# Optimization experiments

Hardware: AMD Instinct MI355X
Metric: run time of the kernel (lower is better)

## Reference

```python
import jax, jax.numpy as jnp
import numpy as np

K_NEIGHBORS = 16
BN_EPS = 1e-5


def _bn(h, g, b):
    # train-mode BatchNorm1d over (batch, points) per channel, biased variance
    mu = h.mean(axis=(0, 1))
    var = h.var(axis=(0, 1))
    return g * (h - mu) * jax.lax.rsqrt(var + BN_EPS) + b


def _gather(arr, idx):
    # arr: [B,N,D], idx: [B,N,K] -> [B,N,K,D]
    return jax.vmap(lambda a, i: a[i])(arr, idx)


def setup_inputs() -> dict:
    key = jax.random.key(0)
    ks = jax.random.split(key, 16)
    B, N, Cin, C, H, M = 4, 4096, 64, 64, 32, 4
    rn = lambda k, s: jax.random.normal(k, s, dtype=jnp.float32) * 0.05
    return {
        "x": jax.random.normal(ks[0], (B, N, Cin), dtype=jnp.float32),
        "p": jax.random.normal(ks[1], (B, N, 3), dtype=jnp.float32),
        "fc1_w": rn(ks[2], (Cin, C)), "fc1_b": jnp.zeros((C,), jnp.float32),
        "bn1_g": jnp.ones((C,), jnp.float32), "bn1_b": jnp.zeros((C,), jnp.float32),
        "qkv_w": rn(ks[3], (C, 3 * C)),
        "pos_w1": rn(ks[4], (3, H)), "pos_b1": jnp.zeros((H,), jnp.float32),
        "pos_w2": rn(ks[5], (H, C)), "pos_b2": jnp.zeros((C,), jnp.float32),
        "attn_w1": rn(ks[6], (C, M * C)), "attn_b1": jnp.zeros((M * C,), jnp.float32),
        "attn_w2": rn(ks[7], (M * C, C)), "attn_b2": jnp.zeros((C,), jnp.float32),
        "bn2_g": jnp.ones((C,), jnp.float32), "bn2_b": jnp.zeros((C,), jnp.float32),
        "fc2_w": rn(ks[8], (C, C)), "fc2_b": jnp.zeros((C,), jnp.float32),
        "bn3_g": jnp.ones((C,), jnp.float32), "bn3_b": jnp.zeros((C,), jnp.float32),
    }


def reference(x, p, fc1_w, fc1_b, bn1_g, bn1_b, qkv_w,
              pos_w1, pos_b1, pos_w2, pos_b2,
              attn_w1, attn_b1, attn_w2, attn_b2,
              bn2_g, bn2_b, fc2_w, fc2_b, bn3_g, bn3_b):
    C = fc1_w.shape[1]
    # fc1 -> BN -> ReLU
    h = jax.nn.relu(_bn(x @ fc1_w + fc1_b, bn1_g, bn1_b))
    residual = h

    # PointTransformerLayer (vector attention over kNN; mask is all-ones)
    qkv = h @ qkv_w  # [B,N,3C]
    q, k, v = qkv[..., :C], qkv[..., C:2 * C], qkv[..., 2 * C:]
    # squared pairwise distances (matches norm-based topk ranking)
    sq = jnp.sum(p * p, axis=-1)  # [B,N]
    d2 = sq[:, :, None] + sq[:, None, :] - 2.0 * jnp.einsum('bnd,bmd->bnm', p, p)
    _, idx = jax.lax.top_k(-d2, K_NEIGHBORS)  # k smallest distances, [B,N,K]

    kj = _gather(k, idx)          # [B,N,K,C]
    vj = _gather(v, idx)          # [B,N,K,C]
    pj = _gather(p, idx)          # [B,N,K,3]

    rel_pos = p[:, :, None, :] - pj                      # [B,N,K,3]
    pe = jax.nn.relu(rel_pos @ pos_w1 + pos_b1) @ pos_w2 + pos_b2  # [B,N,K,C]

    qk_rel = q[:, :, None, :] - kj                       # [B,N,K,C]
    vv = vj + pe
    sim = jax.nn.relu((qk_rel + pe) @ attn_w1 + attn_b1) @ attn_w2 + attn_b2
    attn = jax.nn.softmax(sim, axis=2)                   # softmax over neighbors
    agg = jnp.sum(attn * vv, axis=2)                     # [B,N,C]

    h2 = jax.nn.relu(_bn(agg, bn2_g, bn2_b))
    y = jax.nn.relu(_bn((h2 + residual) @ fc2_w + fc2_b, bn3_g, bn3_b))
    return (y, p)
```

## Files before the change

kernel.cpp:

```cpp
#include <hip/hip_runtime.h>
#include <math.h>

constexpr int kB = 4, kN = 4096, kK = 16;
constexpr int kRows = kB * kN;
constexpr float kEps = 1e-5f;
constexpr float kFltMax = 3.402823466e38f;
constexpr int kCap = 240;

typedef __attribute__((ext_vector_type(8))) short short8;
typedef __attribute__((ext_vector_type(4))) float f32x4;

__device__ __forceinline__ unsigned short f2bf(float x) {
  return (unsigned short)((__float_as_uint(x) + 0x8000u) >> 16);
}
__device__ __forceinline__ unsigned int pkbf(float lo, float hi) {
  return ((__float_as_uint(lo) + 0x8000u) >> 16) |
         ((__float_as_uint(hi) + 0x8000u) & 0xffff0000u);
}
__device__ __forceinline__ short8 pack8f(float4 a, float4 b) {
  union { unsigned int u[4]; short8 s; } pk;
  pk.u[0] = pkbf(a.x, a.y);
  pk.u[1] = pkbf(a.z, a.w);
  pk.u[2] = pkbf(b.x, b.y);
  pk.u[3] = pkbf(b.z, b.w);
  return pk.s;
}

__device__ __forceinline__ int lane_prefix(unsigned long long m) {
  return __builtin_amdgcn_mbcnt_hi((unsigned)(m >> 32),
         __builtin_amdgcn_mbcnt_lo((unsigned)m, 0));
}

__device__ __forceinline__ void bitonic64(float& sv, int& si, int lane) {
  #pragma unroll
  for (int k = 2; k <= 64; k <<= 1) {
    #pragma unroll
    for (int j = k >> 1; j > 0; j >>= 1) {
      float ov = __shfl_xor(sv, j);
      int   oi = __shfl_xor(si, j);
      bool up = ((lane & k) == 0);
      bool lower = ((lane & j) == 0);
      bool osm = (ov < sv) || (ov == sv && oi < si);
      bool take = (lower == up) ? osm : !osm;
      if (take) { sv = ov; si = oi; }
    }
  }
}

__global__ __launch_bounds__(256) void fc1_conv_kernel(
    const float* __restrict__ x, const float* __restrict__ w,
    const float* __restrict__ bias,
    const float* __restrict__ aw1, const float* __restrict__ aw2,
    const float* __restrict__ pw2, const float* __restrict__ qw,
    const float* __restrict__ f2w,
    const float* __restrict__ pin, float* __restrict__ p4o,
    unsigned short* __restrict__ wpak,
    float* __restrict__ out) {
  __shared__ unsigned short wf[8 * 512];
  const int t = threadIdx.x;
  const int blk = blockIdx.x;
  {
    int id = blk * 256 + t;
    if (id < 16384) {
      int j = id & 7, lane = (id >> 3) & 63, rest = id >> 9;
      int mt = rest >> 1, hh = rest & 1;
      wpak[id] = f2bf(aw1[(32 * hh + 8 * (lane >> 4) + j) * 256 + mt * 16 + (lane & 15)]);
      float3 pp = *reinterpret_cast<const float3*>(pin + 3 * id);
      float4 o;
      o.x = pp.x; o.y = pp.y; o.z = pp.z;
      o.w = pp.x * pp.x + pp.y * pp.y + pp.z * pp.z;
      *reinterpret_cast<float4*>(p4o + 4 * id) = o;
    } else if (id < 32768) {
      int i = id - 16384;
      int j = i & 7, lane = (i >> 3) & 63, rest = i >> 9;
      int ct = rest >> 3, f = rest & 7;
      wpak[id] = f2bf(aw2[(32 * f + 8 * (lane >> 4) + j) * 64 + ct * 16 + (lane & 15)]);
    } else if (id < 34816) {
      int i = id - 32768;
      int c = i >> 5, hh = i & 31;
      wpak[id] = f2bf(pw2[hh * 64 + c]);
    } else if (id < 47104) {
      int i = id - 34816;
      int j = i & 7, lane = (i >> 3) & 63, rest = i >> 9;
      int ct = rest >> 1, hh = rest & 1;
      wpak[id] = f2bf(qw[(32 * hh + 8 * (lane >> 4) + j) * 192 + ct * 16 + (lane & 15)]);
    } else if (id < 51200) {
      int i = id - 47104;
      int j = i & 7, lane = (i >> 3) & 63, rest = i >> 9;
      int ct = rest >> 1, hh = rest & 1;
      wpak[id] = f2bf(f2w[(32 * hh + 8 * (lane >> 4) + j) * 64 + ct * 16 + (lane & 15)]);
    }
  }
  for (int i = t; i < 4096; i += 256) {
    int j = i & 7, lane = (i >> 3) & 63, rest = i >> 9;
    int ct = rest >> 1, hh = rest & 1;
    wf[i] = f2bf(w[(32 * hh + 8 * (lane >> 4) + j) * 64 + ct * 16 + (lane & 15)]);
  }
  __syncthreads();
  const int lane = t & 63, wv = t >> 6;
  const int l = lane & 15, q = lane >> 4;
  const int r0 = blk * 64;
  const int row = r0 + wv * 16 + l;
  const f32x4 zero = {0.f, 0.f, 0.f, 0.f};
  float4 xa0 = *reinterpret_cast<const float4*>(&x[row * 64 + q * 8]);
  float4 xa1 = *reinterpret_cast<const float4*>(&x[row * 64 + q * 8 + 4]);
  float4 xb0 = *reinterpret_cast<const float4*>(&x[row * 64 + 32 + q * 8]);
  float4 xb1 = *reinterpret_cast<const float4*>(&x[row * 64 + 32 + q * 8 + 4]);
  short8 a0 = pack8f(xa0, xa1), a1 = pack8f(xb0, xb1);
  #pragma unroll
  for (int ct = 0; ct < 4; ++ct) {
    short8 b0 = *reinterpret_cast<const short8*>(&wf[(ct * 2 + 0) * 512 + lane * 8]);
    short8 b1 = *reinterpret_cast<const short8*>(&wf[(ct * 2 + 1) * 512 + lane * 8]);
    f32x4 acc = __builtin_amdgcn_mfma_f32_16x16x32_bf16(a0, b0, zero, 0, 0, 0);
    acc = __builtin_amdgcn_mfma_f32_16x16x32_bf16(a1, b1, acc, 0, 0, 0);
    const float bc = bias[ct * 16 + l];
    #pragma unroll
    for (int i = 0; i < 4; ++i)
      out[(r0 + wv * 16 + q * 4 + i) * 64 + ct * 16 + l] = acc[i] + bc;
  }
}

__global__ void stats_part_kernel(const float* __restrict__ src, float* __restrict__ part) {
  __shared__ float sb[256], sb2[256];
  const int t = threadIdx.x, blk = blockIdx.x;
  const int c = t & 63, rg = t >> 6;
  float s = 0.f, s2 = 0.f;
  for (int r = rg; r < 64; r += 4) {
    float v = src[(blk * 64 + r) * 64 + c];
    s += v; s2 += v * v;
  }
  sb[t] = s; sb2[t] = s2; __syncthreads();
  if (t < 64) {
    float ts  = sb[t] + sb[64 + t] + sb[128 + t] + sb[192 + t];
    float ts2 = sb2[t] + sb2[64 + t] + sb2[128 + t] + sb2[192 + t];
    part[blk * 128 + t] = ts;
    part[blk * 128 + 64 + t] = ts2;
  }
}

__global__ void stats_fin_kernel(const float* __restrict__ part,
                                 const float* __restrict__ g, const float* __restrict__ b,
                                 float* __restrict__ A, float* __restrict__ Bv) {
  const int c = threadIdx.x;
  double s = 0.0, s2 = 0.0;
  for (int i = 0; i < 256; ++i) { s += part[i * 128 + c]; s2 += part[i * 128 + 64 + c]; }
  double mean = s / (double)kRows;
  double var = s2 / (double)kRows - mean * mean;
  float rs = (float)(1.0 / sqrt(var + (double)kEps));
  float Af = g[c] * rs;
  A[c] = Af;
  Bv[c] = b[c] - (float)mean * Af;
}

__global__ __launch_bounds__(256) void qkv_bn_kernel(
    const float* __restrict__ hpre, const float* __restrict__ A1,
    const float* __restrict__ B1, const unsigned short* __restrict__ wqf,
    float* __restrict__ hout, unsigned short* __restrict__ out) {
  const int t = threadIdx.x, lane = t & 63, wv = t >> 6;
  const int l = lane & 15, q = lane >> 4;
  const int r0 = blockIdx.x * 64;
  const int row = r0 + wv * 16 + l;
  const f32x4 zero = {0.f, 0.f, 0.f, 0.f};
  short8 af[2];
  #pragma unroll
  for (int hh = 0; hh < 2; ++hh) {
    const int c0 = 32 * hh + q * 8;
    float4 v0 = *reinterpret_cast<const float4*>(&hpre[row * 64 + c0]);
    float4 v1 = *reinterpret_cast<const float4*>(&hpre[row * 64 + c0 + 4]);
    float4 Aa = *reinterpret_cast<const float4*>(&A1[c0]);
    float4 Ab = *reinterpret_cast<const float4*>(&A1[c0 + 4]);
    float4 Ba = *reinterpret_cast<const float4*>(&B1[c0]);
    float4 Bb = *reinterpret_cast<const float4*>(&B1[c0 + 4]);
    v0.x = fmaxf(Aa.x * v0.x + Ba.x, 0.f); v0.y = fmaxf(Aa.y * v0.y + Ba.y, 0.f);
    v0.z = fmaxf(Aa.z * v0.z + Ba.z, 0.f); v0.w = fmaxf(Aa.w * v0.w + Ba.w, 0.f);
    v1.x = fmaxf(Ab.x * v1.x + Bb.x, 0.f); v1.y = fmaxf(Ab.y * v1.y + Bb.y, 0.f);
    v1.z = fmaxf(Ab.z * v1.z + Bb.z, 0.f); v1.w = fmaxf(Ab.w * v1.w + Bb.w, 0.f);
    *reinterpret_cast<float4*>(&hout[row * 64 + c0]) = v0;
    *reinterpret_cast<float4*>(&hout[row * 64 + c0 + 4]) = v1;
    af[hh] = pack8f(v0, v1);
  }
  #pragma unroll
  for (int ct = 0; ct < 12; ++ct) {
    short8 b0 = *reinterpret_cast<const short8*>(&wqf[((ct * 2 + 0) * 64 + lane) * 8]);
    short8 b1 = *reinterpret_cast<const short8*>(&wqf[((ct * 2 + 1) * 64 + lane) * 8]);
    f32x4 acc = __builtin_amdgcn_mfma_f32_16x16x32_bf16(af[0], b0, zero, 0, 0, 0);
    acc = __builtin_amdgcn_mfma_f32_16x16x32_bf16(af[1], b1, acc, 0, 0, 0);
    #pragma unroll
    for (int i = 0; i < 4; ++i)
      out[(r0 + wv * 16 + q * 4 + i) * 192 + ct * 16 + l] = f2bf(acc[i]);
  }
}

__global__ __launch_bounds__(256) void knn_attn_kernel(
    const float* __restrict__ p4, const unsigned short* __restrict__ qkv,
    const float* __restrict__ pos_w1, const float* __restrict__ pos_b1,
    const float* __restrict__ pos_b2,
    const float* __restrict__ attn_b1, const float* __restrict__ attn_b2,
    const unsigned short* __restrict__ w1f,
    const unsigned short* __restrict__ w2f,
    const unsigned short* __restrict__ pw2t,
    float* __restrict__ agg) {
  __shared__ unsigned short Ulds[64 * 72];
  __shared__ float VVlds[64 * 68];
  __shared__ int   knnidx[4][kCap];

  const int t = threadIdx.x;
  const int lane = t & 63, w = t >> 6;
  const int l = lane & 15, q = lane >> 4;
  const int work = ((blockIdx.x & 7) << 9) | (blockIdx.x >> 3);
  const int b = work >> 10;
  const int pt_row = work * 4 + w;
  const int base = b * kN;
  const f32x4 zero = {0.f, 0.f, 0.f, 0.f};

  int* bufi = knnidx[w];

  const float4 qp4 = *reinterpret_cast<const float4*>(p4 + 4 * pt_row);
  const float qx = qp4.x, qy = qp4.y, qz = qp4.z, sqq = qp4.w;

  float d2r[16];
  float lmin = kFltMax;
  #pragma unroll
  for (int i = 0; i < 16; ++i) {
    float4 c = *reinterpret_cast<const float4*>(p4 + 4 * (base + i * 64 + lane));
    float dot = fmaf(qz, c.z, fmaf(qy, c.y, qx * c.x));
    float d2 = fmaf(-2.0f, dot, sqq + c.w);
    d2r[i] = d2;
    lmin = fminf(lmin, d2);
  }
  { int dummy = lane; bitonic64(lmin, dummy, lane); }
  const float thrA = __shfl(lmin, 15) + 1e-3f;

  int cntv = 0;
  #pragma unroll
  for (int i = 0; i < 16; ++i) {
    bool qual = d2r[i] <= thrA;
    unsigned long long m = __ballot(qual);
    if (qual) {
      int pos = cntv + lane_prefix(m);
      if (pos < kCap) bufi[pos] = i * 64 + lane;
    }
    cntv += __popcll(m);
  }
  for (int c0 = 16; c0 < 64; c0 += 8) {
    float4 cc[8];
    #pragma unroll
    for (int j = 0; j < 8; ++j)
      cc[j] = *reinterpret_cast<const float4*>(p4 + 4 * (base + (c0 + j) * 64 + lane));
    #pragma unroll
    for (int j = 0; j < 8; ++j) {
      float dot = fmaf(qz, cc[j].z, fmaf(qy, cc[j].y, qx * cc[j].x));
      float d2 = fmaf(-2.0f, dot, sqq + cc[j].w);
      bool qual = d2 <= thrA;
      unsigned long long m = __ballot(qual);
      if (qual) {
        int pos = cntv + lane_prefix(m);
        if (pos < kCap) bufi[pos] = (c0 + j) * 64 + lane;
      }
      cntv += __popcll(m);
    }
  }

  const int n = cntv;
  float sv = kFltMax;
  int   si = 0x7fffffff;
  if (n <= kCap) {
    for (int g0 = 0; g0 < n; g0 += 48) {
      float mv; int mi;
      if (lane < 16) { mv = sv; mi = si; }
      else {
        int pos = g0 + (lane - 16);
        if (pos < n) {
          int jj = bufi[pos];
          float4 c = *reinterpret_cast<const float4*>(p4 + 4 * (base + jj));
          float dot = fmaf(qz, c.z, fmaf(qy, c.y, qx * c.x));
          mv = fmaf(-2.0f, dot, sqq + c.w);
          mi = jj;
        } else { mv = kFltMax; mi = 0x7fffffff; }
      }
      bitonic64(mv, mi, lane);
      sv = mv; si = mi;
    }
  } else {
    for (int g0 = 0; g0 < kN; g0 += 48) {
      float mv; int mi;
      if (lane < 16) { mv = sv; mi = si; }
      else {
        int j = g0 + (lane - 16);
        if (j < kN) {
          float4 c = *reinterpret_cast<const float4*>(p4 + 4 * (base + j));
          float dot = fmaf(qz, c.z, fmaf(qy, c.y, qx * c.x));
          mv = fmaf(-2.0f, dot, sqq + c.w);
          mi = j;
        } else { mv = kFltMax; mi = 0x7fffffff; }
      }
      bitonic64(mv, mi, lane);
      sv = mv; si = mi;
    }
  }

  int idxv = 0;
  if (lane < 16) {
    int o = si;
    if ((unsigned)o >= (unsigned)kN) o = 0;
    idxv = o;
  }

  {
    const int r = lane >> 2, seg = lane & 3;
    const unsigned short* jrow = qkv + (base + __shfl(idxv, r)) * 192;
    const int c0 = seg * 16;
    uint4 k0 = *reinterpret_cast<const uint4*>(jrow + 64 + c0);
    uint4 k1 = *reinterpret_cast<const uint4*>(jrow + 64 + c0 + 8);
    uint4 v0 = *reinterpret_cast<const uint4*>(jrow + 128 + c0);
    uint4 v1 = *reinterpret_cast<const uint4*>(jrow + 128 + c0 + 8);
    uint4 q0 = *reinterpret_cast<const uint4*>(qkv + pt_row * 192 + c0);
    uint4 q1 = *reinterpret_cast<const uint4*>(qkv + pt_row * 192 + c0 + 8);
    auto diff2 = [](unsigned int qu, unsigned int ku) -> unsigned int {
      float lo = __uint_as_float(qu << 16) - __uint_as_float(ku << 16);
      float hi = __uint_as_float(qu & 0xffff0000u) - __uint_as_float(ku & 0xffff0000u);
      return pkbf(lo, hi);
    };
    uint4 u0, u1;
    u0.x = diff2(q0.x, k0.x); u0.y = diff2(q0.y, k0.y);
    u0.z = diff2(q0.z, k0.z); u0.w = diff2(q0.w, k0.w);
    u1.x = diff2(q1.x, k1.x); u1.y = diff2(q1.y, k1.y);
    u1.z = diff2(q1.z, k1.z); u1.w = diff2(q1.w, k1.w);
    *reinterpret_cast<uint4*>(&Ulds[(w * 16 + r) * 72 + c0]) = u0;
    *reinterpret_cast<uint4*>(&Ulds[(w * 16 + r) * 72 + c0 + 8]) = u1;
    const unsigned int vs[8] = {v0.x, v0.y, v0.z, v0.w, v1.x, v1.y, v1.z, v1.w};
    #pragma unroll
    for (int i = 0; i < 4; ++i) {
      float4 vv;
      vv.x = __uint_as_float(vs[2 * i] << 16);
      vv.y = __uint_as_float(vs[2 * i] & 0xffff0000u);
      vv.z = __uint_as_float(vs[2 * i + 1] << 16);
      vv.w = __uint_as_float(vs[2 * i + 1] & 0xffff0000u);
      *reinterpret_cast<float4*>(&VVlds[(w * 16 + r) * 68 + c0 + 4 * i]) = vv;
    }
  }
  short8 pbf;
  {
    const int nj = __shfl(idxv, l);
    const float4 pj4 = *reinterpret_cast<const float4*>(p4 + 4 * (base + nj));
    float rx = qx - pj4.x, ry = qy - pj4.y, rz = qz - pj4.z;
    float hv[8];
    #pragma unroll
    for (int j = 0; j < 8; ++j) {
      int hh = q * 8 + j;
      hv[j] = fmaxf(pos_b1[hh] + rx * pos_w1[hh] + ry * pos_w1[32 + hh] +
                    rz * pos_w1[64 + hh], 0.0f);
    }
    union { unsigned int u[4]; short8 s; } pk;
    #pragma unroll
    for (int ii = 0; ii < 4; ++ii) pk.u[ii] = pkbf(hv[2 * ii], hv[2 * ii + 1]);
    pbf = pk.s;
  }

  {
    const int urow = (w * 16 + l) * 72;
    const int vrow = (w * 16 + l) * 68;
    #pragma unroll
    for (int mt = 0; mt < 4; ++mt) {
      short8 paf = *reinterpret_cast<const short8*>(&pw2t[(mt * 16 + l) * 32 + q * 8]);
      f32x4 pe = __builtin_amdgcn_mfma_f32_16x16x32_bf16(paf, pbf, zero, 0, 0, 0);
      const int c0 = mt * 16 + q * 4;
      float4 b2v = *reinterpret_cast<const float4*>(&pos_b2[c0]);
      float pe0 = pe[0] + b2v.x, pe1 = pe[1] + b2v.y;
      float pe2 = pe[2] + b2v.z, pe3 = pe[3] + b2v.w;
      uint2 u2 = *reinterpret_cast<uint2*>(&Ulds[urow + c0]);
      uint2 o;
      o.x = pkbf(__uint_as_float(u2.x << 16) + pe0,
                 __uint_as_float(u2.x & 0xffff0000u) + pe1);
      o.y = pkbf(__uint_as_float(u2.y << 16) + pe2,
                 __uint_as_float(u2.y & 0xffff0000u) + pe3);
      *reinterpret_cast<uint2*>(&Ulds[urow + c0]) = o;
      float4 vv = *reinterpret_cast<float4*>(&VVlds[vrow + c0]);
      vv.x += pe0; vv.y += pe1; vv.z += pe2; vv.w += pe3;
      *reinterpret_cast<float4*>(&VVlds[vrow + c0]) = vv;
    }
  }

  unsigned int plo[16], phi[16];
  {
    const int urow = (w * 16 + l) * 72;
    short8 ub0 = *reinterpret_cast<const short8*>(&Ulds[urow + q * 8]);
    short8 ub1 = *reinterpret_cast<const short8*>(&Ulds[urow + 32 + q * 8]);
    #pragma unroll
    for (int mt = 0; mt < 16; ++mt) {
      short8 a0 = *reinterpret_cast<const short8*>(&w1f[(mt * 2 + 0) * 512 + lane * 8]);
      short8 a1 = *reinterpret_cast<const short8*>(&w1f[(mt * 2 + 1) * 512 + lane * 8]);
      f32x4 acc = __builtin_amdgcn_mfma_f32_16x16x32_bf16(a0, ub0, zero, 0, 0, 0);
      acc = __builtin_amdgcn_mfma_f32_16x16x32_bf16(a1, ub1, acc, 0, 0, 0);
      float4 bb = *reinterpret_cast<const float4*>(&attn_b1[mt * 16 + q * 4]);
      plo[mt] = pkbf(fmaxf(acc[0] + bb.x, 0.f), fmaxf(acc[1] + bb.y, 0.f));
      phi[mt] = pkbf(fmaxf(acc[2] + bb.z, 0.f), fmaxf(acc[3] + bb.w, 0.f));
    }
  }

  {
    f32x4 acc2[4];
    #pragma unroll
    for (int ct = 0; ct < 4; ++ct) acc2[ct] = zero;
    const int sbase = l + 32 * (q & 1);
    const bool hi_mt = (q >= 2);
    #pragma unroll
    for (int f = 0; f < 8; ++f) {
      union { unsigned int u[4]; short8 s; } pk;
      #pragma unroll
      for (int d = 0; d < 4; ++d) {
        const int src = sbase + ((d >> 1) << 4);
        const unsigned int w0 = (d & 1) ? phi[2 * f] : plo[2 * f];
        const unsigned int w1v = (d & 1) ? phi[2 * f + 1] : plo[2 * f + 1];
        unsigned int va = (unsigned int)__shfl((int)w0, src);
        unsigned int vb = (unsigned int)__shfl((int)w1v, src);
        pk.u[d] = hi_mt ? vb : va;
      }
      short8 afr = pk.s;
      #pragma unroll
      for (int ct = 0; ct < 4; ++ct) {
        short8 bfr = *reinterpret_cast<const short8*>(&w2f[((ct * 8 + f) * 64 + lane) * 8]);
        acc2[ct] = __builtin_amdgcn_mfma_f32_16x16x32_bf16(afr, bfr, acc2[ct], 0, 0, 0);
      }
    }
    #pragma unroll
    for (int ct = 0; ct < 4; ++ct) {
      const int ch = ct * 16 + l;
      const float bv = attn_b2[ch];
      float s0v = acc2[ct][0] + bv, s1v = acc2[ct][1] + bv;
      float s2v = acc2[ct][2] + bv, s3v = acc2[ct][3] + bv;
      float mx = fmaxf(fmaxf(s0v, s1v), fmaxf(s2v, s3v));
      mx = fmaxf(mx, __shfl_xor(mx, 16, 64));
      mx = fmaxf(mx, __shfl_xor(mx, 32, 64));
      float e0 = __expf(s0v - mx), e1 = __expf(s1v - mx);
      float e2 = __expf(s2v - mx), e3 = __expf(s3v - mx);
      float se = e0 + e1 + e2 + e3;
      se += __shfl_xor(se, 16, 64);
      se += __shfl_xor(se, 32, 64);
      const int vbase = (w * 16 + q * 4) * 68 + ch;
      float a = e0 * VVlds[vbase] + e1 * VVlds[vbase + 68] +
                e2 * VVlds[vbase + 136] + e3 * VVlds[vbase + 204];
      a += __shfl_xor(a, 16, 64);
      a += __shfl_xor(a, 32, 64);
      if (q == 0) agg[pt_row * 64 + ch] = a / se;
    }
  }
}

__global__ __launch_bounds__(256) void fc2_mfma_kernel(
    const float* __restrict__ aggp, const float* __restrict__ hres,
    const float* __restrict__ A2, const float* __restrict__ B2,
    const unsigned short* __restrict__ fc2f, const float* __restrict__ bias,
    float* __restrict__ z) {
  const int t = threadIdx.x, lane = t & 63, wv = t >> 6;
  const int l = lane & 15, q = lane >> 4;
  const int r0 = blockIdx.x * 64;
  const int row = r0 + wv * 16 + l;
  const f32x4 zero = {0.f, 0.f, 0.f, 0.f};
  short8 af[2];
  #pragma unroll
  for (int hh = 0; hh < 2; ++hh) {
    const int c0 = 32 * hh + q * 8;
    float4 v0 = *reinterpret_cast<const float4*>(&aggp[row * 64 + c0]);
    float4 v1 = *reinterpret_cast<const float4*>(&aggp[row * 64 + c0 + 4]);
    float4 r0v = *reinterpret_cast<const float4*>(&hres[row * 64 + c0]);
    float4 r1v = *reinterpret_cast<const float4*>(&hres[row * 64 + c0 + 4]);
    float4 Aa = *reinterpret_cast<const float4*>(&A2[c0]);
    float4 Ab = *reinterpret_cast<const float4*>(&A2[c0 + 4]);
    float4 Ba = *reinterpret_cast<const float4*>(&B2[c0]);
    float4 Bb = *reinterpret_cast<const float4*>(&B2[c0 + 4]);
    v0.x = fmaxf(Aa.x * v0.x + Ba.x, 0.f) + r0v.x;
    v0.y = fmaxf(Aa.y * v0.y + Ba.y, 0.f) + r0v.y;
    v0.z = fmaxf(Aa.z * v0.z + Ba.z, 0.f) + r0v.z;
    v0.w = fmaxf(Aa.w * v0.w + Ba.w, 0.f) + r0v.w;
    v1.x = fmaxf(Ab.x * v1.x + Bb.x, 0.f) + r1v.x;
    v1.y = fmaxf(Ab.y * v1.y + Bb.y, 0.f) + r1v.y;
    v1.z = fmaxf(Ab.z * v1.z + Bb.z, 0.f) + r1v.z;
    v1.w = fmaxf(Ab.w * v1.w + Bb.w, 0.f) + r1v.w;
    af[hh] = pack8f(v0, v1);
  }
  #pragma unroll
  for (int ct = 0; ct < 4; ++ct) {
    short8 b0 = *reinterpret_cast<const short8*>(&fc2f[((ct * 2 + 0) * 64 + lane) * 8]);
    short8 b1 = *reinterpret_cast<const short8*>(&fc2f[((ct * 2 + 1) * 64 + lane) * 8]);
    f32x4 acc = __builtin_amdgcn_mfma_f32_16x16x32_bf16(af[0], b0, zero, 0, 0, 0);
    acc = __builtin_amdgcn_mfma_f32_16x16x32_bf16(af[1], b1, acc, 0, 0, 0);
    const float bc = bias[ct * 16 + l];
    #pragma unroll
    for (int i = 0; i < 4; ++i)
      z[(r0 + wv * 16 + q * 4 + i) * 64 + ct * 16 + l] = acc[i] + bc;
  }
}

__global__ void final_kernel(const float* __restrict__ z, const float* __restrict__ A3,
                             const float* __restrict__ B3, const float* __restrict__ p,
                             float* __restrict__ y) {
  const int blk = blockIdx.x, t = threadIdx.x;
  if (blk < 4096) {
    int i = blk * 256 + t;
    int c = i & 63;
    y[i] = fmaxf(A3[c] * z[i] + B3[c], 0.0f);
  } else {
    int i = (blk - 4096) * 256 + t;
    y[1048576 + i] = p[i];
  }
}

extern "C" void kernel_launch(void* const* d_in, const int* in_sizes, int n_in,
                              void* d_out, int out_size, void* d_ws, size_t ws_size,
                              hipStream_t stream) {
  const float* x       = (const float*)d_in[0];
  const float* p       = (const float*)d_in[1];
  const float* fc1_w   = (const float*)d_in[2];
  const float* fc1_b   = (const float*)d_in[3];
  const float* bn1_g   = (const float*)d_in[4];
  const float* bn1_b   = (const float*)d_in[5];
  const float* qkv_w   = (const float*)d_in[6];
  const float* pos_w1  = (const float*)d_in[7];
  const float* pos_b1  = (const float*)d_in[8];
  const float* pos_w2  = (const float*)d_in[9];
  const float* pos_b2  = (const float*)d_in[10];
  const float* attn_w1 = (const float*)d_in[11];
  const float* attn_b1 = (const float*)d_in[12];
  const float* attn_w2 = (const float*)d_in[13];
  const float* attn_b2 = (const float*)d_in[14];
  const float* bn2_g   = (const float*)d_in[15];
  const float* bn2_b   = (const float*)d_in[16];
  const float* fc2_w   = (const float*)d_in[17];
  const float* fc2_b   = (const float*)d_in[18];
  const float* bn3_g   = (const float*)d_in[19];
  const float* bn3_b   = (const float*)d_in[20];

  float* ws   = (float*)d_ws;
  float* h    = ws;
  unsigned short* qkvb = (unsigned short*)(ws + 1048576);
  float* hpre = ws + 4194304;
  float* aggv = ws + 5242880;
  float* z    = ws + 6291456;
  float* st   = ws + 7340032;
  float* p4   = ws + 7356800;
  unsigned short* wpak = (unsigned short*)(ws + 7618944);
  unsigned short* w1f  = wpak;
  unsigned short* w2f  = wpak + 16384;
  unsigned short* pw2t = wpak + 32768;
  unsigned short* wqf  = wpak + 34816;
  unsigned short* fc2f = wpak + 47104;

  float* A1 = st,       *B1 = st + 64;
  float* A2 = st + 128, *B2 = st + 192;
  float* A3 = st + 256, *B3 = st + 320;
  float* y = (float*)d_out;

  fc1_conv_kernel<<<256, 256, 0, stream>>>(x, fc1_w, fc1_b, attn_w1, attn_w2,
                                           pos_w2, qkv_w, fc2_w, p, p4, wpak, hpre);
  stats_part_kernel<<<256, 256, 0, stream>>>(hpre, aggv);
  stats_fin_kernel<<<1, 64, 0, stream>>>(aggv, bn1_g, bn1_b, A1, B1);
  qkv_bn_kernel<<<256, 256, 0, stream>>>(hpre, A1, B1, wqf, h, qkvb);
  knn_attn_kernel<<<4096, 256, 0, stream>>>(p4, qkvb, pos_w1, pos_b1, pos_b2,
                                            attn_b1, attn_b2, w1f, w2f, pw2t, aggv);
  stats_part_kernel<<<256, 256, 0, stream>>>(aggv, z);
  stats_fin_kernel<<<1, 64, 0, stream>>>(z, bn2_g, bn2_b, A2, B2);
  fc2_mfma_kernel<<<256, 256, 0, stream>>>(aggv, h, A2, B2, fc2f, fc2_b, z);
  stats_part_kernel<<<256, 256, 0, stream>>>(z, aggv);
  stats_fin_kernel<<<1, 64, 0, stream>>>(aggv, bn3_g, bn3_b, A3, B3);
  final_kernel<<<4288, 256, 0, stream>>>(z, A3, B3, p, y);
}
```

Baseline: 284.0 us.

## Share kNN candidate scan across block waves, building per-query lists cooperatively

Each wave now loads only a quarter of the batch's points and computes distances to all four queries in the block. It keeps bf16-truncated distances in registers, and the per-wave thresholds are exchanged through shared memory. Candidate lists are then appended with LDS atomics into reused VVlds space. This cuts the redundant per-wave global loads of the whole point cloud by four times. The trade-off is a looser threshold taken from a subset, which means more candidates to refine and a higher chance of overflowing the cap. It also adds extra syncs and atomics.

```diff
diff --git a/kernel.cpp b/kernel.cpp
--- a/kernel.cpp
+++ b/kernel.cpp
@@ -202,7 +202,8 @@
     float* __restrict__ agg) {
   __shared__ unsigned short Ulds[64 * 72];
   __shared__ float VVlds[64 * 68];
-  __shared__ int   knnidx[4][kCap];
+  __shared__ int   scnt[4];
+  __shared__ float sthr[4];
 
   const int t = threadIdx.x;
   const int lane = t & 63, w = t >> 6;
@@ -210,58 +211,99 @@
   const int work = ((blockIdx.x & 7) << 9) | (blockIdx.x >> 3);
   const int b = work >> 10;
   const int pt_row = work * 4 + w;
+  const int qrow0 = work * 4;
   const int base = b * kN;
   const f32x4 zero = {0.f, 0.f, 0.f, 0.f};
 
-  int* bufi = knnidx[w];
-
+  if (t < 4) scnt[t] = 0;
+
+  const float4 q0f = *reinterpret_cast<const float4*>(p4 + 4 * (qrow0 + 0));
+  const float4 q1f = *reinterpret_cast<const float4*>(p4 + 4 * (qrow0 + 1));
+  const float4 q2f = *reinterpret_cast<const float4*>(p4 + 4 * (qrow0 + 2));
+  const float4 q3f = *reinterpret_cast<const float4*>(p4 + 4 * (qrow0 + 3));
   const float4 qp4 = *reinterpret_cast<const float4*>(p4 + 4 * pt_row);
   const float qx = qp4.x, qy = qp4.y, qz = qp4.z, sqq = qp4.w;
 
-  float d2r[16];
+  auto d2q = [](const float4& Q, const float4& C) -> float {
+    float dt = fmaf(Q.z, C.z, fmaf(Q.y, C.y, Q.x * C.x));
+    return fmaf(-2.0f, dt, Q.w + C.w);
+  };
+  unsigned pk0[8], pk1[8], pk2[8], pk3[8];
   float lmin = kFltMax;
+  const int cbase = base + w * 1024;
   #pragma unroll
-  for (int i = 0; i < 16; ++i) {
-    float4 c = *reinterpret_cast<const float4*>(p4 + 4 * (base + i * 64 + lane));
-    float dot = fmaf(qz, c.z, fmaf(qy, c.y, qx * c.x));
-    float d2 = fmaf(-2.0f, dot, sqq + c.w);
-    d2r[i] = d2;
-    lmin = fminf(lmin, d2);
-  }
-  { int dummy = lane; bitonic64(lmin, dummy, lane); }
-  const float thrA = __shfl(lmin, 15) + 1e-3f;
-
-  int cntv = 0;
-  #pragma unroll
-  for (int i = 0; i < 16; ++i) {
-    bool qual = d2r[i] <= thrA;
-    unsigned long long m = __ballot(qual);
-    if (qual) {
-      int pos = cntv + lane_prefix(m);
-      if (pos < kCap) bufi[pos] = i * 64 + lane;
-    }
-    cntv += __popcll(m);
-  }
-  for (int c0 = 16; c0 < 64; c0 += 8) {
+  for (int g = 0; g < 2; ++g) {
     float4 cc[8];
     #pragma unroll
-    for (int j = 0; j < 8; ++j)
-      cc[j] = *reinterpret_cast<const float4*>(p4 + 4 * (base + (c0 + j) * 64 + lane));
-    #pragma unroll
-    for (int j = 0; j < 8; ++j) {
-      float dot = fmaf(qz, cc[j].z, fmaf(qy, cc[j].y, qx * cc[j].x));
-      float d2 = fmaf(-2.0f, dot, sqq + cc[j].w);
-      bool qual = d2 <= thrA;
-      unsigned long long m = __ballot(qual);
-      if (qual) {
-        int pos = cntv + lane_prefix(m);
-        if (pos < kCap) bufi[pos] = (c0 + j) * 64 + lane;
+    for (int jj = 0; jj < 8; ++jj)
+      cc[jj] = *reinterpret_cast<const float4*>(p4 + 4 * (cbase + (g * 8 + jj) * 64 + lane));
+    #pragma unroll
+    for (int jj = 0; jj < 8; ++jj) {
+      float dot = fmaf(qz, cc[jj].z, fmaf(qy, cc[jj].y, qx * cc[jj].x));
+      lmin = fminf(lmin, fmaf(-2.0f, dot, sqq + cc[jj].w));
+    }
+    #pragma unroll
+    for (int pi = 0; pi < 4; ++pi) {
+      const float4 ca = cc[2 * pi], cb = cc[2 * pi + 1];
+      pk0[g * 4 + pi] = (__float_as_uint(d2q(q0f, ca)) >> 16) |
+                        (__float_as_uint(d2q(q0f, cb)) & 0xffff0000u);
+      pk1[g * 4 + pi] = (__float_as_uint(d2q(q1f, ca)) >> 16) |
+                        (__float_as_uint(d2q(q1f, cb)) & 0xffff0000u);
+      pk2[g * 4 + pi] = (__float_as_uint(d2q(q2f, ca)) >> 16) |
+                        (__float_as_uint(d2q(q2f, cb)) & 0xffff0000u);
+      pk3[g * 4 + pi] = (__float_as_uint(d2q(q3f, ca)) >> 16) |
+                        (__float_as_uint(d2q(q3f, cb)) & 0xffff0000u);
+    }
+  }
+  {
+    int dummy = lane;
+    float lm = lmin;
+    bitonic64(lm, dummy, lane);
+    float s16 = __shfl(lm, 15);
+    if (lane == 0) sthr[w] = s16 + 1e-3f;
+  }
+  __syncthreads();
+
+  {
+    auto append_q = [&](const unsigned (&PK)[8], int j) {
+      int* listj = reinterpret_cast<int*>(VVlds + j * 1088);
+      const float thrj = sthr[j];
+      #pragma unroll
+      for (int g = 0; g < 2; ++g) {
+        unsigned long long m[8];
+        int pc[8];
+        #pragma unroll
+        for (int c = 0; c < 8; ++c) {
+          unsigned pku = PK[g * 4 + (c >> 1)];
+          float dv = (c & 1) ? __uint_as_float(pku & 0xffff0000u)
+                             : __uint_as_float(pku << 16);
+          m[c] = __ballot(dv <= thrj);
+          pc[c] = __popcll(m[c]);
+        }
+        int tot = pc[0] + pc[1] + pc[2] + pc[3] + pc[4] + pc[5] + pc[6] + pc[7];
+        int old = 0;
+        if (lane == 0) old = atomicAdd(&scnt[j], tot);
+        old = __shfl(old, 0);
+        int pre = 0;
+        #pragma unroll
+        for (int c = 0; c < 8; ++c) {
+          if ((m[c] >> lane) & 1ull) {
+            int pos = old + pre + lane_prefix(m[c]);
+            if (pos < kCap) listj[pos] = w * 1024 + (g * 8 + c) * 64 + lane;
+          }
+          pre += pc[c];
+        }
       }
-      cntv += __popcll(m);
-    }
-  }
-
-  const int n = cntv;
+    };
+    append_q(pk0, 0);
+    append_q(pk1, 1);
+    append_q(pk2, 2);
+    append_q(pk3, 3);
+  }
+  __syncthreads();
+
+  const int n = scnt[w];
+  int* bufi = reinterpret_cast<int*>(VVlds + w * 1088);
   float sv = kFltMax;
   int   si = 0x7fffffff;
   if (n <= kCap) {
@@ -305,6 +347,8 @@
     if ((unsigned)o >= (unsigned)kN) o = 0;
     idxv = o;
   }
+
+  asm volatile("" ::: "memory");
 
   {
     const int r = lane >> 2, seg = lane & 3;
```

Result: no change. 288.4 us (+1.5%).
